# Performance work log

Hardware: AMD Instinct MI355X
Metric: run time of the kernel (lower is better)

The kernel has to match this reference:

```python
import jax, jax.numpy as jnp
import numpy as np

B, P, K = 32, 2048, 32  # clouds, points per cloud, max_num_neighbors


def _pairwise_sqdist(pos):  # [P,3] -> [P,P]
    d = pos[:, None, :] - pos[None, :, :]
    return jnp.sum(d * d, axis=-1)


def _radius_neighbors(pos, r, k):
    """For each point, up to k nearest neighbors within radius r (no self),
    plus an always-valid self-loop slot (PointNetConv add_self_loops=True)."""
    n = pos.shape[0]
    d2 = _pairwise_sqdist(pos)
    mask = (d2 <= r * r) & (~jnp.eye(n, dtype=bool))
    score = jnp.where(mask, d2, jnp.inf)
    neg, idx = jax.lax.top_k(-score, k)        # k nearest within radius
    valid = neg > -jnp.inf
    idx = jnp.concatenate([idx, jnp.arange(n)[:, None]], axis=1)  # [P,k+1]
    valid = jnp.concatenate([valid, jnp.ones((n, 1), bool)], axis=1)
    return idx, valid


def _point_conv(x, pos, idx, valid, W1, b1, W2, b2):
    """max_j local_nn(concat(x_j, pos_j - pos_i)) over neighbors j of i."""
    rel = pos[idx] - pos[:, None, :]           # [P,k+1,3]
    feats = rel if x is None else jnp.concatenate([x[idx], rel], axis=-1)
    h = jax.nn.relu(feats @ W1 + b1) @ W2 + b2  # [P,k+1,C]
    h = jnp.where(valid[:, :, None], h, -jnp.inf)
    return jnp.max(h, axis=1)                  # [P,C]


def _fps_idx(pos, n):
    """Farthest point sampling of n indices, deterministic start at 0."""
    d = jnp.sum((pos - pos[0]) ** 2, axis=-1)

    def body(d, _):
        i = jnp.argmax(d)
        di = jnp.sum((pos - pos[i]) ** 2, axis=-1)
        return jnp.minimum(d, di), i

    _, idxs = jax.lax.scan(body, d, None, length=n - 1)
    return jnp.concatenate([jnp.zeros((1,), idxs.dtype), idxs])


def setup_inputs() -> dict:
    key = jax.random.key(0)
    ks = jax.random.split(key, 16)
    pos = jax.random.uniform(ks[0], (B * P, 3), dtype=jnp.float32)
    batch = jnp.repeat(jnp.arange(B, dtype=jnp.int64), P)

    def lin(k, fi, fo):
        s = 1.0 / np.sqrt(fi)
        kw, kb = jax.random.split(k)
        return (jax.random.uniform(kw, (fi, fo), jnp.float32, -s, s),
                jax.random.uniform(kb, (fo,), jnp.float32, -s, s))

    W1a, b1a = lin(ks[1], 3, 64)
    W1b, b1b = lin(ks[2], 64, 64)
    W2a, b2a = lin(ks[3], 67, 128)
    W2b, b2b = lin(ks[4], 128, 128)
    W3a, b3a = lin(ks[5], 131, 256)
    W3b, b3b = lin(ks[6], 256, 256)
    Wl1, bl1 = lin(ks[7], 256, 256)
    Wl2, bl2 = lin(ks[8], 256, 256)
    Wl3, bl3 = lin(ks[9], 256, 40)
    return dict(pos=pos, batch=batch,
                W1a=W1a, b1a=b1a, W1b=W1b, b1b=b1b,
                W2a=W2a, b2a=b2a, W2b=W2b, b2b=b2b,
                W3a=W3a, b3a=b3a, W3b=W3b, b3b=b3b,
                Wl1=Wl1, bl1=bl1, Wl2=Wl2, bl2=bl2, Wl3=Wl3, bl3=bl3)


def reference(pos, batch, W1a, b1a, W1b, b1b, W2a, b2a, W2b, b2b,
              W3a, b3a, W3b, b3b, Wl1, bl1, Wl2, bl2, Wl3, bl3):
    pos3 = pos.reshape(B, P, 3)  # batch is uniform: repeat(arange(B), P)

    def per_cloud(p):
        idx, valid = _radius_neighbors(p, 0.2, K)
        x = jax.nn.relu(_point_conv(None, p, idx, valid, W1a, b1a, W1b, b1b))
        s = _fps_idx(p, P // 2)
        x, p = x[s], p[s]
        idx, valid = _radius_neighbors(p, 0.4, K)
        x = jax.nn.relu(_point_conv(x, p, idx, valid, W2a, b2a, W2b, b2b))
        s = _fps_idx(p, P // 8)
        x, p = x[s], p[s]
        idx, valid = _radius_neighbors(p, 1.0, K)
        x = jax.nn.relu(_point_conv(x, p, idx, valid, W3a, b3a, W3b, b3b))
        return jnp.max(x, axis=0)  # global max pool per cloud

    g = jax.vmap(per_cloud)(pos3)                     # [B,256]
    h = jax.nn.relu(g @ Wl1 + bl1)
    h = jax.nn.relu(h @ Wl2 + bl2)                    # dropout is identity in eval
    return jax.nn.log_softmax(h @ Wl3 + bl3, axis=-1)  # [B,40]
```

## Files before the change

kernel.cpp:

```cpp
#include <hip/hip_runtime.h>
#include <math.h>

#define DEV static __device__ __forceinline__

typedef short s8v  __attribute__((ext_vector_type(8)));
typedef short s4v  __attribute__((ext_vector_type(4)));
typedef float f4v  __attribute__((ext_vector_type(4)));

DEV short bf16rne(float f) {
    unsigned u = __float_as_uint(f);
    unsigned r = (u + 0x7fffu + ((u >> 16) & 1u)) >> 16;
    return (short)r;
}

DEV float sqd(float ax, float ay, float az, float bx, float by, float bz) {
    float dx = __fsub_rn(ax, bx), dy = __fsub_rn(ay, by), dz = __fsub_rn(az, bz);
    return __fadd_rn(__fadd_rn(__fmul_rn(dx, dx), __fmul_rn(dy, dy)), __fmul_rn(dz, dz));
}

template <int CTRL, int ROWMASK>
DEV void dpp_min_step(unsigned long long& k) {
    unsigned klo = (unsigned)k, khi = (unsigned)(k >> 32);
    int olo = __builtin_amdgcn_update_dpp((int)klo, (int)klo, CTRL, ROWMASK, 0xF, false);
    int ohi = __builtin_amdgcn_update_dpp((int)khi, (int)khi, CTRL, ROWMASK, 0xF, false);
    unsigned long long ok = (((unsigned long long)(unsigned)ohi) << 32) | (unsigned)olo;
    k = (ok < k) ? ok : k;
}

DEV unsigned long long dpp_wave_min_bcast(unsigned long long k) {
    dpp_min_step<0xB1,  0xF>(k);
    dpp_min_step<0x4E,  0xF>(k);
    dpp_min_step<0x141, 0xF>(k);
    dpp_min_step<0x140, 0xF>(k);
    dpp_min_step<0x142, 0xA>(k);
    dpp_min_step<0x143, 0xC>(k);
    unsigned glo = (unsigned)__builtin_amdgcn_readlane((int)(unsigned)k, 63);
    unsigned ghi = (unsigned)__builtin_amdgcn_readlane((int)(unsigned)(k >> 32), 63);
    return (((unsigned long long)ghi) << 32) | glo;
}

template <int CTRL, int ROWMASK>
DEV void fps_dpp_step(unsigned long long& k, float& bx, float& by, float& bz) {
    unsigned klo = (unsigned)k, khi = (unsigned)(k >> 32);
    int olo = __builtin_amdgcn_update_dpp((int)klo, (int)klo, CTRL, ROWMASK, 0xF, false);
    int ohi = __builtin_amdgcn_update_dpp((int)khi, (int)khi, CTRL, ROWMASK, 0xF, false);
    int oxi = __builtin_amdgcn_update_dpp(__float_as_int(bx), __float_as_int(bx), CTRL, ROWMASK, 0xF, false);
    int oyi = __builtin_amdgcn_update_dpp(__float_as_int(by), __float_as_int(by), CTRL, ROWMASK, 0xF, false);
    int ozi = __builtin_amdgcn_update_dpp(__float_as_int(bz), __float_as_int(bz), CTRL, ROWMASK, 0xF, false);
    unsigned long long ok = (((unsigned long long)(unsigned)ohi) << 32) | (unsigned)olo;
    bool take = ok > k;
    k  = take ? ok : k;
    bx = take ? __int_as_float(oxi) : bx;
    by = take ? __int_as_float(oyi) : by;
    bz = take ? __int_as_float(ozi) : bz;
}

DEV void fps_wave_argmax(unsigned long long& k, float& bx, float& by, float& bz) {
    fps_dpp_step<0xB1,  0xF>(k, bx, by, bz);
    fps_dpp_step<0x4E,  0xF>(k, bx, by, bz);
    fps_dpp_step<0x141, 0xF>(k, bx, by, bz);
    fps_dpp_step<0x140, 0xF>(k, bx, by, bz);
    fps_dpp_step<0x142, 0xA>(k, bx, by, bz);
    fps_dpp_step<0x143, 0xC>(k, bx, by, bz);
}

template <int N, int CAP>
DEV void radius_wave(const float* __restrict__ p, float rr, int b, int i,
                     int lane, unsigned long long* __restrict__ buf,
                     int* __restrict__ idx_out) {
    constexpr int Q = N / 64;
    constexpr int RREGS = CAP / 64;
    constexpr unsigned long long INV = ~0ull;
    float qx = p[i * 3 + 0], qy = p[i * 3 + 1], qz = p[i * 3 + 2];
    int* orow = idx_out + ((size_t)b * N + i) * 33;

#pragma unroll
    for (int t = 0; t < RREGS; t++) buf[t * 64 + lane] = INV;

    bool ovf = false;
    int base = 0;
    for (int q = 0; q < Q; q++) {
        int jj = q * 64 + lane;
        float d2 = sqd(p[jj * 3 + 0], p[jj * 3 + 1], p[jj * 3 + 2], qx, qy, qz);
        bool valid = (jj != i) && (d2 <= rr);
        unsigned long long mask = __ballot(valid);
        int tot = __popcll(mask);
        if (base + tot > CAP) { ovf = true; break; }
        if (valid) {
            unsigned mlo = (unsigned)mask, mhi = (unsigned)(mask >> 32);
            int pre = __builtin_amdgcn_mbcnt_hi(mhi, __builtin_amdgcn_mbcnt_lo(mlo, 0));
            buf[base + pre] = (((unsigned long long)__float_as_uint(d2)) << 32)
                              | (unsigned)jj;
        }
        base += tot;
    }

    if (!ovf) {
        unsigned long long r[RREGS];
#pragma unroll
        for (int t = 0; t < RREGS; t++) r[t] = buf[t * 64 + lane];
        int cnt = 0;
        for (int s = 0; s < 32; s++) {
            unsigned long long m = r[0];
#pragma unroll
            for (int t = 1; t < RREGS; t++) m = (r[t] < m) ? r[t] : m;
            unsigned long long g = dpp_wave_min_bcast(m);
            if (g == INV) break;
            if (lane == 0) orow[cnt] = (int)(unsigned)(g & 0xffffffffull);
            cnt++;
#pragma unroll
            for (int t = 0; t < RREGS; t++) r[t] = (r[t] == g) ? INV : r[t];
        }
        if (cnt < 32) {
            for (int t2 = cnt + 1 + lane; t2 < 33; t2 += 64) orow[t2] = -1;
            if (lane == 0) orow[cnt] = i;
        } else {
            if (lane == 0) orow[32] = i;
        }
        return;
    }

    unsigned long long c[Q];
#pragma unroll
    for (int q = 0; q < Q; q++) {
        int jj = q * 64 + lane;
        float d2 = sqd(p[jj * 3 + 0], p[jj * 3 + 1], p[jj * 3 + 2], qx, qy, qz);
        bool valid = (jj != i) && (d2 <= rr);
        c[q] = valid ? ((((unsigned long long)__float_as_uint(d2)) << 32)
                        | (unsigned)jj)
                     : INV;
    }
#pragma unroll
    for (int k = 2; k <= Q; k <<= 1) {
#pragma unroll
        for (int jj = k >> 1; jj > 0; jj >>= 1) {
#pragma unroll
            for (int t = 0; t < Q; t++) {
                int l = t ^ jj;
                if (l > t) {
                    bool up = ((t & k) == 0);
                    unsigned long long a = c[t], d = c[l];
                    bool sw = (a > d) != up;
                    c[t] = sw ? d : a;
                    c[l] = sw ? a : d;
                }
            }
        }
    }
    int cnt = 0;
    for (int s = 0; s < 32; s++) {
        unsigned long long h = c[0];
        unsigned long long g = dpp_wave_min_bcast(h);
        if (lane == 0) orow[s] = (int)(unsigned)(g & 0xffffffffull);
        cnt += (g != INV) ? 1 : 0;
        if (h == g && g != INV) {
#pragma unroll
            for (int q = 0; q < Q - 1; q++) c[q] = c[q + 1];
            c[Q - 1] = INV;
        }
    }
    if (lane == 0) {
        if (cnt < 32) orow[cnt] = i;
        orow[32] = (cnt == 32) ? i : -1;
    }
}

template <int N, int M, int CAP>
__global__ __launch_bounds__(256) void radius_fps_kernel(
        const float* __restrict__ pos, float rr, int* __restrict__ idx_out,
        int* __restrict__ s_out) {
    constexpr size_t FPS_BYTES = 192 + (size_t)M * 4;
    constexpr size_t RAD_BYTES = (size_t)4 * CAP * 8;
    constexpr size_t SMEM = (FPS_BYTES > RAD_BYTES) ? FPS_BYTES : RAD_BYTES;
    __shared__ __align__(16) char smem[SMEM];
    int b = blockIdx.x;
    const float* p = pos + (size_t)b * N * 3;

    if (blockIdx.y == N / 4) {
        unsigned long long (*wkey)[4] = (unsigned long long (*)[4])smem;
        float (*wxyz)[4][4] = (float (*)[4][4])(smem + 64);
        int* swin = (int*)(smem + 192);
        constexpr int P = N / 256;
        int tid = threadIdx.x;
        int w = tid >> 6, lane = tid & 63;
        float cx[P], cy[P], cz[P], d[P];
#pragma unroll
        for (int q = 0; q < P; q++) {
            int j = q * 256 + tid;
            cx[q] = p[j * 3 + 0];
            cy[q] = p[j * 3 + 1];
            cz[q] = p[j * 3 + 2];
            d[q] = INFINITY;
        }
        float sx = p[0], sy = p[1], sz = p[2];
        if (tid == 0) swin[0] = 0;
#pragma unroll 1
        for (int m = 1; m < M; m++) {
            float best = -INFINITY, bx = 0.f, by = 0.f, bz = 0.f;
            int bj = 0;
#pragma unroll
            for (int q = 0; q < P; q++) {
                float di = sqd(cx[q], cy[q], cz[q], sx, sy, sz);
                float dn = fminf(d[q], di);
                d[q] = dn;
                bool take = dn > best;
                best = take ? dn : best;
                bj = take ? (q * 256 + tid) : bj;
                bx = take ? cx[q] : bx;
                by = take ? cy[q] : by;
                bz = take ? cz[q] : bz;
            }
            unsigned long long key =
                (((unsigned long long)__float_as_uint(best)) << 32)
                | (unsigned)(0xFFFFFFFFu - (unsigned)bj);
            fps_wave_argmax(key, bx, by, bz);
            int par = m & 1;
            if (lane == 63) {
                wkey[par][w] = key;
                f4v cv; cv[0] = bx; cv[1] = by; cv[2] = bz; cv[3] = 0.f;
                *(f4v*)&wxyz[par][w][0] = cv;
            }
            __syncthreads();
            unsigned long long k0 = wkey[par][0], k1 = wkey[par][1];
            unsigned long long k2 = wkey[par][2], k3 = wkey[par][3];
            f4v c0 = *(const f4v*)&wxyz[par][0][0];
            f4v c1 = *(const f4v*)&wxyz[par][1][0];
            f4v c2 = *(const f4v*)&wxyz[par][2][0];
            f4v c3 = *(const f4v*)&wxyz[par][3][0];
            bool a01 = k1 > k0;
            unsigned long long k01 = a01 ? k1 : k0;
            f4v c01 = a01 ? c1 : c0;
            bool a23 = k3 > k2;
            unsigned long long k23 = a23 ? k3 : k2;
            f4v c23 = a23 ? c3 : c2;
            bool af = k23 > k01;
            unsigned long long kf = af ? k23 : k01;
            f4v cf = af ? c23 : c01;
            sx = cf[0]; sy = cf[1]; sz = cf[2];
            if (tid == 0)
                swin[m] = (int)(0xFFFFFFFFu - (unsigned)(kf & 0xFFFFFFFFull));
        }
        __syncthreads();
        int* so = s_out + b * M;
        for (int j = tid; j < M; j += 256) so[j] = swin[j];
        return;
    }

    int wid = threadIdx.x >> 6, lane = threadIdx.x & 63;
    int i = blockIdx.y * 4 + wid;
    unsigned long long* buf = ((unsigned long long*)smem) + (size_t)wid * CAP;
    radius_wave<N, CAP>(p, rr, b, i, lane, buf, idx_out);
}

template <int N, int CAP>
__global__ __launch_bounds__(256) void radius_topk_kernel(
        const float* __restrict__ pos, float rr, int* __restrict__ idx_out) {
    __shared__ __align__(16) unsigned long long buf4[4 * CAP];
    int b = blockIdx.x;
    int wid = threadIdx.x >> 6, lane = threadIdx.x & 63;
    int i = blockIdx.y * 4 + wid;
    const float* p = pos + (size_t)b * N * 3;
    radius_wave<N, CAP>(p, rr, b, i, lane, buf4 + (size_t)wid * CAP, idx_out);
}

__global__ void pack_w_kernel(const float* __restrict__ W, short* __restrict__ out,
                              int Kreal, int C, int KS, int total) {
    int t = blockIdx.x * 256 + threadIdx.x;
    if (t >= total) return;
    int lane = t & 63;
    int mk = t >> 6;
    int ks = mk % KS, mt = mk / KS;
    int c = 16 * mt + (lane & 15);
    int k0 = 32 * ks + ((lane >> 4) << 3);
    s8v v;
#pragma unroll
    for (int j = 0; j < 8; j++) {
        int k = k0 + j;
        v[j] = (k < Kreal) ? bf16rne(W[(size_t)k * C + c]) : (short)0;
    }
    *(s8v*)(out + (size_t)t * 8) = v;
}

template <int CXIN, int CH, int PPB, int N>
__global__ __launch_bounds__(256) void conv_mfma_kernel(
        const float* __restrict__ pos, const float* __restrict__ xin,
        const int* __restrict__ idx,
        const short* __restrict__ Wpa, const float* __restrict__ ba,
        const short* __restrict__ Wpb, const float* __restrict__ bb,
        float* __restrict__ xout) {
    constexpr int CIN  = CXIN + 3;
    constexpr int CINp = (CIN + 31) & ~31;
    constexpr int KS1  = CINp / 32, KS2 = CH / 32;
    constexpr int MT   = CH / 16;
    constexpr int MTW  = (PPB == 4) ? MT : MT / 4;
    constexpr int RP   = 48;
    constexpr int NT   = 3;
    constexpr int FS   = CINp * 2 + 16;
    constexpr int HS   = CH * 2 + 16;
    __shared__ __align__(16) char Fs[PPB * RP * FS];
    __shared__ __align__(16) char Hs[PPB * RP * HS];
    __shared__ int sj[PPB * RP];

    int tid = threadIdx.x;
    int lane = tid & 63, wid = tid >> 6;
    int pid0 = blockIdx.x * PPB;

    for (int r = tid; r < PPB * RP; r += 256) {
        int p = r / RP, s = r - p * RP;
        sj[r] = (s < 33) ? idx[(size_t)(pid0 + p) * 33 + s] : -1;
    }
    __syncthreads();

    constexpr int FE = PPB * RP * CINp;
    for (int e = tid; e < FE; e += 256) {
        int r = e / CINp, f = e - r * CINp;
        int p = r / RP;
        int pid = pid0 + p;
        int b = pid / N, i = pid - b * N;
        int j = sj[r];
        float v = 0.f;
        if (j >= 0 && f < CIN) {
            if (f < CXIN) {
                v = xin[((size_t)b * N + j) * CXIN + f];
            } else {
                int a = f - CXIN;
                v = __fsub_rn(pos[((size_t)b * N + j) * 3 + a],
                              pos[((size_t)b * N + i) * 3 + a]);
            }
        }
        *(short*)(Fs + (size_t)r * FS + f * 2) = bf16rne(v);
    }
    __syncthreads();

    int pw  = (PPB == 4) ? wid : 0;
    int mt0 = (PPB == 4) ? 0 : wid * MTW;
    const char* Fw = Fs + pw * RP * FS;
    char* Hw = Hs + pw * RP * HS;
    int lr = lane & 15, lg = lane >> 4;

    f4v acc[MTW][NT];
#pragma unroll
    for (int m = 0; m < MTW; m++)
#pragma unroll
        for (int nt = 0; nt < NT; nt++)
#pragma unroll
            for (int q = 0; q < 4; q++) acc[m][nt][q] = 0.f;
#pragma unroll
    for (int ks = 0; ks < KS1; ks++) {
        s8v bfr[NT];
#pragma unroll
        for (int nt = 0; nt < NT; nt++)
            bfr[nt] = *(const s8v*)(Fw + (nt * 16 + lr) * FS + (32 * ks + lg * 8) * 2);
#pragma unroll
        for (int m = 0; m < MTW; m++) {
            s8v afr = *(const s8v*)(Wpa + (((size_t)(mt0 + m) * KS1 + ks) * 64 + lane) * 8);
#pragma unroll
            for (int nt = 0; nt < NT; nt++)
                acc[m][nt] = __builtin_amdgcn_mfma_f32_16x16x32_bf16(afr, bfr[nt], acc[m][nt], 0, 0, 0);
        }
    }
#pragma unroll
    for (int m = 0; m < MTW; m++) {
        int cbase = (mt0 + m) * 16 + lg * 4;
        f4v bv = *(const f4v*)(ba + cbase);
#pragma unroll
        for (int nt = 0; nt < NT; nt++) {
            s4v hq;
#pragma unroll
            for (int q = 0; q < 4; q++)
                hq[q] = bf16rne(fmaxf(acc[m][nt][q] + bv[q], 0.f));
            *(s4v*)(Hw + (nt * 16 + lr) * HS + cbase * 2) = hq;
        }
    }
    __syncthreads();

    f4v acc2[MTW][NT];
#pragma unroll
    for (int m = 0; m < MTW; m++)
#pragma unroll
        for (int nt = 0; nt < NT; nt++)
#pragma unroll
            for (int q = 0; q < 4; q++) acc2[m][nt][q] = 0.f;
#pragma unroll
    for (int ks = 0; ks < KS2; ks++) {
        s8v bfr[NT];
#pragma unroll
        for (int nt = 0; nt < NT; nt++)
            bfr[nt] = *(const s8v*)(Hw + (nt * 16 + lr) * HS + (32 * ks + lg * 8) * 2);
#pragma unroll
        for (int m = 0; m < MTW; m++) {
            s8v afr = *(const s8v*)(Wpb + (((size_t)(mt0 + m) * KS2 + ks) * 64 + lane) * 8);
#pragma unroll
            for (int nt = 0; nt < NT; nt++)
                acc2[m][nt] = __builtin_amdgcn_mfma_f32_16x16x32_bf16(afr, bfr[nt], acc2[m][nt], 0, 0, 0);
        }
    }

    const int* sjw = sj + pw * RP;
#pragma unroll
    for (int m = 0; m < MTW; m++) {
        int cbase = (mt0 + m) * 16 + lg * 4;
        f4v bv = *(const f4v*)(bb + cbase);
        f4v vmx;
#pragma unroll
        for (int q = 0; q < 4; q++) vmx[q] = 0.f;
#pragma unroll
        for (int nt = 0; nt < NT; nt++) {
            int s = nt * 16 + lr;
            bool valid = (s < 33) && (sjw[s] >= 0);
#pragma unroll
            for (int q = 0; q < 4; q++) {
                float v = fmaxf(acc2[m][nt][q] + bv[q], 0.f);
                if (valid) vmx[q] = fmaxf(vmx[q], v);
            }
        }
#pragma unroll
        for (int off = 1; off < 16; off <<= 1)
#pragma unroll
            for (int q = 0; q < 4; q++)
                vmx[q] = fmaxf(vmx[q], __shfl_xor(vmx[q], off, 64));
        if (lr == 0) {
            int pid = pid0 + pw;
            *(f4v*)(xout + (size_t)pid * CH + cbase) = vmx;
        }
    }
}

__global__ void gather_kernel(
        const float* __restrict__ pos_in, const float* __restrict__ x_in,
        const int* __restrict__ s, int Nin, int M, int C,
        float* __restrict__ pos_out, float* __restrict__ x_out) {
    int b = blockIdx.y, m = blockIdx.x, t = threadIdx.x;
    int j = s[b * M + m];
    x_out[((size_t)b * M + m) * C + t] = x_in[((size_t)b * Nin + j) * C + t];
    if (t < 3) pos_out[((size_t)b * M + m) * 3 + t] = pos_in[((size_t)b * Nin + j) * 3 + t];
}

__global__ __launch_bounds__(256) void head_kernel(
        const float* __restrict__ x3,
        const float* __restrict__ Wl1, const float* __restrict__ bl1,
        const float* __restrict__ Wl2, const float* __restrict__ bl2,
        const float* __restrict__ Wl3, const float* __restrict__ bl3,
        float* __restrict__ out) {
    __shared__ float gbuf[256], h1[256], h2[256], h3[40];
    int b = blockIdx.x, c = threadIdx.x;
    const float* xb = x3 + (size_t)b * 256 * 256;
    float m = -INFINITY;
    for (int r = 0; r < 256; r++) m = fmaxf(m, xb[r * 256 + c]);
    gbuf[c] = m;
    __syncthreads();
    float a = bl1[c];
    for (int k = 0; k < 256; k++) a = fmaf(gbuf[k], Wl1[k * 256 + c], a);
    h1[c] = fmaxf(a, 0.f);
    __syncthreads();
    a = bl2[c];
    for (int k = 0; k < 256; k++) a = fmaf(h1[k], Wl2[k * 256 + c], a);
    h2[c] = fmaxf(a, 0.f);
    __syncthreads();
    if (c < 40) {
        a = bl3[c];
        for (int k = 0; k < 256; k++) a = fmaf(h2[k], Wl3[k * 40 + c], a);
        h3[c] = a;
    }
    __syncthreads();
    if (c < 64) {
        float v = -INFINITY;
        if (c < 40) v = h3[c];
        float mx = v;
#pragma unroll
        for (int off = 32; off >= 1; off >>= 1) mx = fmaxf(mx, __shfl_xor(mx, off, 64));
        float e = (c < 40) ? expf(__fsub_rn(v, mx)) : 0.f;
        float s = e;
#pragma unroll
        for (int off = 32; off >= 1; off >>= 1) s = __fadd_rn(s, __shfl_xor(s, off, 64));
        float ls = logf(s);
        if (c < 40) out[b * 40 + c] = __fsub_rn(__fsub_rn(v, mx), ls);
    }
}

extern "C" void kernel_launch(void* const* d_in, const int* in_sizes, int n_in,
                              void* d_out, int out_size, void* d_ws, size_t ws_size,
                              hipStream_t stream) {
    (void)in_sizes; (void)n_in; (void)out_size; (void)ws_size;
    const float* pos = (const float*)d_in[0];
    const float* W1a = (const float*)d_in[2];
    const float* b1a = (const float*)d_in[3];
    const float* W1b = (const float*)d_in[4];
    const float* b1b = (const float*)d_in[5];
    const float* W2a = (const float*)d_in[6];
    const float* b2a = (const float*)d_in[7];
    const float* W2b = (const float*)d_in[8];
    const float* b2b = (const float*)d_in[9];
    const float* W3a = (const float*)d_in[10];
    const float* b3a = (const float*)d_in[11];
    const float* W3b = (const float*)d_in[12];
    const float* b3b = (const float*)d_in[13];
    const float* Wl1 = (const float*)d_in[14];
    const float* bl1 = (const float*)d_in[15];
    const float* Wl2 = (const float*)d_in[16];
    const float* bl2 = (const float*)d_in[17];
    const float* Wl3 = (const float*)d_in[18];
    const float* bl3 = (const float*)d_in[19];
    float* out = (float*)d_out;

    const int B = 32;
    char* w = (char*)d_ws;
    auto alloc = [&](size_t bytes) -> char* {
        char* r = w;
        w += (bytes + 255) & ~(size_t)255;
        return r;
    };
    int*   idx1 = (int*)  alloc((size_t)B * 2048 * 33 * 4);
    float* x1   = (float*)alloc((size_t)B * 2048 * 64 * 4);
    int*   s1   = (int*)  alloc((size_t)B * 1024 * 4);
    float* pos2 = (float*)alloc((size_t)B * 1024 * 3 * 4);
    float* x2in = (float*)alloc((size_t)B * 1024 * 64 * 4);
    int*   idx2 = (int*)  alloc((size_t)B * 1024 * 33 * 4);
    float* x2   = (float*)alloc((size_t)B * 1024 * 128 * 4);
    int*   s2   = (int*)  alloc((size_t)B * 256 * 4);
    float* pos3 = (float*)alloc((size_t)B * 256 * 3 * 4);
    float* x3in = (float*)alloc((size_t)B * 256 * 128 * 4);
    int*   idx3 = (int*)  alloc((size_t)B * 256 * 33 * 4);
    float* x3   = (float*)alloc((size_t)B * 256 * 256 * 4);
    short* Wp1a = (short*)alloc(4  * 1 * 64 * 8 * 2);
    short* Wp1b = (short*)alloc(4  * 2 * 64 * 8 * 2);
    short* Wp2a = (short*)alloc(8  * 3 * 64 * 8 * 2);
    short* Wp2b = (short*)alloc(8  * 4 * 64 * 8 * 2);
    short* Wp3a = (short*)alloc(16 * 5 * 64 * 8 * 2);
    short* Wp3b = (short*)alloc(16 * 8 * 64 * 8 * 2);

    pack_w_kernel<<<1,  256, 0, stream>>>(W1a, Wp1a, 3,   64,  1, 256);
    pack_w_kernel<<<2,  256, 0, stream>>>(W1b, Wp1b, 64,  64,  2, 512);
    pack_w_kernel<<<6,  256, 0, stream>>>(W2a, Wp2a, 67,  128, 3, 1536);
    pack_w_kernel<<<8,  256, 0, stream>>>(W2b, Wp2b, 128, 128, 4, 2048);
    pack_w_kernel<<<20, 256, 0, stream>>>(W3a, Wp3a, 131, 256, 5, 5120);
    pack_w_kernel<<<32, 256, 0, stream>>>(W3b, Wp3b, 256, 256, 8, 8192);

    radius_fps_kernel<2048, 1024, 256><<<dim3(B, 513), 256, 0, stream>>>(
        pos, 0.04f, idx1, s1);
    conv_mfma_kernel<0, 64, 4, 2048><<<B * 2048 / 4, 256, 0, stream>>>(
        pos, nullptr, idx1, Wp1a, b1a, Wp1b, b1b, x1);
    gather_kernel<<<dim3(1024, B), 64, 0, stream>>>(pos, x1, s1, 2048, 1024, 64, pos2, x2in);

    radius_fps_kernel<1024, 256, 512><<<dim3(B, 257), 256, 0, stream>>>(
        pos2, 0.16f, idx2, s2);
    conv_mfma_kernel<64, 128, 1, 1024><<<B * 1024, 256, 0, stream>>>(
        pos2, x2in, idx2, Wp2a, b2a, Wp2b, b2b, x2);
    gather_kernel<<<dim3(256, B), 128, 0, stream>>>(pos2, x2, s2, 1024, 256, 128, pos3, x3in);

    radius_topk_kernel<256, 256><<<dim3(B, 64), 256, 0, stream>>>(pos3, 1.0f, idx3);
    conv_mfma_kernel<128, 256, 1, 256><<<B * 256, 256, 0, stream>>>(
        pos3, x3in, idx3, Wp3a, b3a, Wp3b, b3b, x3);

    head_kernel<<<B, 256, 0, stream>>>(x3, Wl1, bl1, Wl2, bl2, Wl3, bl3, out);
}
```

Before: 2.231 ms.

## Run FPS on a single wavefront to remove per-iteration block barriers

The farthest-point-sampling block now uses only one 64-lane wavefront holding N/64 points per lane instead of four waves. Each iteration broadcasts the winner with readlane and writes it straight to global memory, so the shared-memory exchange and __syncthreads are gone. The aim is to cut barrier and LDS latency from the long serial FPS loop, at the cost of four times more serial distance work per lane. Launch bounds are also changed to (256,1), which may alter register allocation and occupancy for the radius blocks that share this kernel.

```diff
diff --git a/kernel.cpp b/kernel.cpp
--- a/kernel.cpp
+++ b/kernel.cpp
@@ -166,34 +166,29 @@
 }
 
 template <int N, int M, int CAP>
-__global__ __launch_bounds__(256) void radius_fps_kernel(
+__global__ __launch_bounds__(256, 1) void radius_fps_kernel(
         const float* __restrict__ pos, float rr, int* __restrict__ idx_out,
         int* __restrict__ s_out) {
-    constexpr size_t FPS_BYTES = 192 + (size_t)M * 4;
-    constexpr size_t RAD_BYTES = (size_t)4 * CAP * 8;
-    constexpr size_t SMEM = (FPS_BYTES > RAD_BYTES) ? FPS_BYTES : RAD_BYTES;
-    __shared__ __align__(16) char smem[SMEM];
+    __shared__ __align__(16) unsigned long long rbuf[4 * CAP];
     int b = blockIdx.x;
     const float* p = pos + (size_t)b * N * 3;
 
     if (blockIdx.y == N / 4) {
-        unsigned long long (*wkey)[4] = (unsigned long long (*)[4])smem;
-        float (*wxyz)[4][4] = (float (*)[4][4])(smem + 64);
-        int* swin = (int*)(smem + 192);
-        constexpr int P = N / 256;
-        int tid = threadIdx.x;
-        int w = tid >> 6, lane = tid & 63;
+        if (threadIdx.x >= 64) return;
+        constexpr int P = N / 64;
+        int lane = threadIdx.x;
         float cx[P], cy[P], cz[P], d[P];
 #pragma unroll
         for (int q = 0; q < P; q++) {
-            int j = q * 256 + tid;
+            int j = q * 64 + lane;
             cx[q] = p[j * 3 + 0];
             cy[q] = p[j * 3 + 1];
             cz[q] = p[j * 3 + 2];
             d[q] = INFINITY;
         }
         float sx = p[0], sy = p[1], sz = p[2];
-        if (tid == 0) swin[0] = 0;
+        int* so = s_out + b * M;
+        if (lane == 0) so[0] = 0;
 #pragma unroll 1
         for (int m = 1; m < M; m++) {
             float best = -INFINITY, bx = 0.f, by = 0.f, bz = 0.f;
@@ -205,7 +200,7 @@
                 d[q] = dn;
                 bool take = dn > best;
                 best = take ? dn : best;
-                bj = take ? (q * 256 + tid) : bj;
+                bj = take ? (q * 64 + lane) : bj;
                 bx = take ? cx[q] : bx;
                 by = take ? cy[q] : by;
                 bz = take ? cz[q] : bz;
@@ -214,42 +209,18 @@
                 (((unsigned long long)__float_as_uint(best)) << 32)
                 | (unsigned)(0xFFFFFFFFu - (unsigned)bj);
             fps_wave_argmax(key, bx, by, bz);
-            int par = m & 1;
-            if (lane == 63) {
-                wkey[par][w] = key;
-                f4v cv; cv[0] = bx; cv[1] = by; cv[2] = bz; cv[3] = 0.f;
-                *(f4v*)&wxyz[par][w][0] = cv;
-            }
-            __syncthreads();
-            unsigned long long k0 = wkey[par][0], k1 = wkey[par][1];
-            unsigned long long k2 = wkey[par][2], k3 = wkey[par][3];
-            f4v c0 = *(const f4v*)&wxyz[par][0][0];
-            f4v c1 = *(const f4v*)&wxyz[par][1][0];
-            f4v c2 = *(const f4v*)&wxyz[par][2][0];
-            f4v c3 = *(const f4v*)&wxyz[par][3][0];
-            bool a01 = k1 > k0;
-            unsigned long long k01 = a01 ? k1 : k0;
-            f4v c01 = a01 ? c1 : c0;
-            bool a23 = k3 > k2;
-            unsigned long long k23 = a23 ? k3 : k2;
-            f4v c23 = a23 ? c3 : c2;
-            bool af = k23 > k01;
-            unsigned long long kf = af ? k23 : k01;
-            f4v cf = af ? c23 : c01;
-            sx = cf[0]; sy = cf[1]; sz = cf[2];
-            if (tid == 0)
-                swin[m] = (int)(0xFFFFFFFFu - (unsigned)(kf & 0xFFFFFFFFull));
-        }
-        __syncthreads();
-        int* so = s_out + b * M;
-        for (int j = tid; j < M; j += 256) so[j] = swin[j];
+            unsigned klo = (unsigned)__builtin_amdgcn_readlane((int)(unsigned)key, 63);
+            sx = __int_as_float(__builtin_amdgcn_readlane(__float_as_int(bx), 63));
+            sy = __int_as_float(__builtin_amdgcn_readlane(__float_as_int(by), 63));
+            sz = __int_as_float(__builtin_amdgcn_readlane(__float_as_int(bz), 63));
+            if (lane == 0) so[m] = (int)(0xFFFFFFFFu - klo);
+        }
         return;
     }
 
     int wid = threadIdx.x >> 6, lane = threadIdx.x & 63;
     int i = blockIdx.y * 4 + wid;
-    unsigned long long* buf = ((unsigned long long*)smem) + (size_t)wid * CAP;
-    radius_wave<N, CAP>(p, rr, b, i, lane, buf, idx_out);
+    radius_wave<N, CAP>(p, rr, b, i, lane, rbuf + (size_t)wid * CAP, idx_out);
 }
 
 template <int N, int CAP>
```

Result: slower. 2.751 ms (+23.3%).
